# Optimization experiments

Hardware: AMD Instinct MI355X
Metric: run time of the kernel (lower is better)

Reference implementation:

```python
import jax, jax.numpy as jnp
import numpy as np

BETA = 0.25  # commitment loss weight (init kwarg)


def setup_inputs() -> dict:
    key = jax.random.key(0)
    k1, k2 = jax.random.split(key)
    z = jax.random.normal(k1, (16, 256, 32, 32), dtype=jnp.float32)
    embedding = jax.random.normal(k2, (8192, 256), dtype=jnp.float32)
    return {"z": z, "embedding": embedding}


def reference(z, embedding):
    # z: [B, C, H, W]  embedding: [K, C]
    B, C, H, W = z.shape
    zp = jnp.transpose(z, (0, 2, 3, 1))            # [B, H, W, C]
    zf = zp.reshape(-1, C)                          # [N, C]
    # squared euclidean distances via ||z||^2 + ||e||^2 - 2 z.e : [N, K]
    d = (jnp.sum(zf * zf, axis=1, keepdims=True)
         + jnp.sum(embedding * embedding, axis=1)
         - 2.0 * jnp.einsum('nd,kd->nk', zf, embedding))
    min_encoding_indices = jnp.argmin(d, axis=1)    # [N]
    z_q = embedding[min_encoding_indices].reshape(zp.shape)  # [B, H, W, C]
    loss = (BETA * jnp.mean((jax.lax.stop_gradient(z_q) - zp) ** 2)
            + jnp.mean((z_q - jax.lax.stop_gradient(zp)) ** 2))
    # straight-through estimator
    z_q = zp + jax.lax.stop_gradient(z_q - zp)
    z_q = jnp.transpose(z_q, (0, 3, 1, 2))          # back to [B, C, H, W]
    return z_q, loss, min_encoding_indices
```

## Files before the change

kernel.cpp:

```cpp
#include <hip/hip_runtime.h>

typedef unsigned int u32;
typedef unsigned long long u64;

#define C_DIM 256
#define HW 1024
#define N_TOT 16384
#define K_DIM 8192
#define ZQ_SIZE 4194304
#define LOSS_OFF ZQ_SIZE
#define IDX_OFF (ZQ_SIZE + 1)

#define KRANGE 2048
#define MARGIN 2.0f
#define CAP 524288u
#define LCAP 4096u

#define WS_ENORM 0
#define WS_CNT 8192
#define WS_PACKED 16384
#define WS_FIDX 49152
#define WS_LPART 65536
#define WS_LIST 131072
#define WS_ZT32 1179648
#define WS_ZTB16 5373952
#define WS_EB16 7471104

typedef __attribute__((ext_vector_type(4))) float f32x4;
typedef __attribute__((ext_vector_type(8))) __bf16 bf16x8;
typedef __attribute__((ext_vector_type(8))) unsigned short u16x8;

__device__ __forceinline__ void gld_lds16(const void* g, void* l) {
    __builtin_amdgcn_global_load_lds(
        (const __attribute__((address_space(1))) u32*)g,
        (__attribute__((address_space(3))) u32*)l, 16, 0, 0);
}

__device__ __forceinline__ unsigned short f2bf(float f) {
    u32 u = __float_as_uint(f);
    u32 r = (u + 0x7FFFu + ((u >> 16) & 1u)) >> 16;
    return (unsigned short)r;
}

__global__ __launch_bounds__(256) void k_prep_e(const float* __restrict__ e,
                                                unsigned short* __restrict__ eb,
                                                float* __restrict__ enorm1) {
    int w = threadIdx.x >> 6, l = threadIdx.x & 63;
    int row = blockIdx.x * 4 + w;
    const float4 v = *reinterpret_cast<const float4*>(e + (size_t)row * C_DIM + l * 4);
    float s = v.x * v.x + v.y * v.y + v.z * v.z + v.w * v.w;
    #pragma unroll
    for (int off = 32; off; off >>= 1) s += __shfl_xor(s, off, 64);
    if (l == 0) enorm1[row] = s + 1024.0f;
    ushort4 h;
    h.x = f2bf(v.x); h.y = f2bf(v.y); h.z = f2bf(v.z); h.w = f2bf(v.w);
    *reinterpret_cast<ushort4*>(eb + (size_t)row * C_DIM + l * 4) = h;
}

__global__ __launch_bounds__(256) void k_prep_z(const float* __restrict__ z,
                                                float* __restrict__ zt32,
                                                unsigned short* __restrict__ ztb) {
    int bid = blockIdx.x;
    int b = bid >> 7;
    int hwt = (bid >> 3) & 15;
    int ct = bid & 7;
    int t = threadIdx.x;
    __shared__ float tile[32][65];
    #pragma unroll
    for (int p = 0; p < 8; ++p) {
        int cl = p * 4 + (t >> 6), hl = t & 63;
        tile[cl][hl] = z[((size_t)b << 18) + ((size_t)(ct * 32 + cl) << 10) + hwt * 64 + hl];
    }
    __syncthreads();
    int hl = t & 63, cg = t >> 6;
    int n = (b << 10) + hwt * 64 + hl;
    float v[8];
    #pragma unroll
    for (int j = 0; j < 8; ++j) v[j] = tile[cg * 8 + j][hl];
    size_t base = (size_t)n * C_DIM + ct * 32 + cg * 8;
    *reinterpret_cast<float4*>(zt32 + base) = make_float4(v[0], v[1], v[2], v[3]);
    *reinterpret_cast<float4*>(zt32 + base + 4) = make_float4(v[4], v[5], v[6], v[7]);
    u16x8 h;
    #pragma unroll
    for (int j = 0; j < 8; ++j) h[j] = f2bf(v[j]);
    *reinterpret_cast<u16x8*>(ztb + base) = h;
}

__global__ __launch_bounds__(256, 1) void k_screen(const unsigned short* __restrict__ zt,
                                                   const unsigned short* __restrict__ et,
                                                   const float* __restrict__ enorm1,
                                                   u32* __restrict__ cnt,
                                                   uint2* __restrict__ list) {
    __shared__ __align__(16) char lds[50704];
    char* Ab2 = lds;
    char* Bb = lds + 32768;

    int logical = (blockIdx.x & 7) * 64 + (blockIdx.x >> 3);
    const int ks = logical >> 7;
    const int rowtile = logical & 127;
    const int n0 = rowtile * 128;
    const int kbase = ks * KRANGE;

    const int tid = threadIdx.x;
    const int l = tid & 63, w = tid >> 6;
    const int wr = w >> 1, wc = w & 1;
    const int ll = l & 15, lh = l >> 4;

    #pragma unroll
    for (int j = 0; j < 8; ++j) {
        int Y = (w * 8 + j) * 1024 + l * 16;
        int row = Y >> 8;
        int slot = (Y >> 4) & 15;
        const char* src = (const char*)zt + (((size_t)(n0 + row)) << 9) + 256
                          + ((slot ^ (row & 7)) << 4);
        gld_lds16(src, Ab2 + (w * 8 + j) * 1024);
    }

    const char* srcB[2];
    char* dstB[2];
    #pragma unroll
    for (int j = 0; j < 2; ++j) {
        int D = w * 128 + j * 64 + l;
        int rB = D >> 2;
        int sB = (D & 3) ^ ((rB >> 1) & 3);
        srcB[j] = (const char*)et + ((size_t)(kbase + rB) << 9) + (sB << 4);
        dstB[j] = Bb + (w * 128 + j * 64) * 16;
    }
    int bfrOff[4];
    #pragma unroll
    for (int kf = 0; kf < 4; ++kf) {
        int row = wc * 64 + kf * 16 + ll;
        bfrOff[kf] = (row * 4 + (lh ^ ((row >> 1) & 3))) * 16;
    }
    int a2off[4], rx2[4];
    #pragma unroll
    for (int mf = 0; mf < 4; ++mf) {
        int row = wr * 64 + mf * 16 + ll;
        a2off[mf] = row * 256;
        rx2[mf] = row & 7;
    }

    gld_lds16(srcB[0], dstB[0]);
    gld_lds16(srcB[1], dstB[1]);

    const char* abase = (const char*)zt + (((size_t)(n0 + wr * 64 + ll)) << 9) + lh * 16;
    bf16x8 afr[4][4];
    #pragma unroll
    for (int mf = 0; mf < 4; ++mf)
        #pragma unroll
        for (int q = 0; q < 4; ++q)
            afr[mf][q] = *reinterpret_cast<const bf16x8*>(abase + mf * 8192 + q * 64);

    f32x4 acc[4][4];
    #pragma unroll
    for (int a = 0; a < 4; ++a)
        #pragma unroll
        for (int b = 0; b < 4; ++b) acc[a][b] = (f32x4){0.f, 0.f, 0.f, 0.f};
    float m1[16], m2[16];
    #pragma unroll
    for (int s = 0; s < 16; ++s) { m1[s] = 3.4e38f; m2[s] = 3.4e38f; }

    __syncthreads();

    for (int it = 0; it < 16; ++it) {
        float en[4];
        #pragma unroll
        for (int kf = 0; kf < 4; ++kf)
            en[kf] = enorm1[kbase + it * 128 + wc * 64 + kf * 16 + ll];

        #pragma unroll
        for (int cs = 0; cs < 8; ++cs) {
            const int p = cs & 1;
            if (it < 15 || cs < 7) {
                const size_t koff = (size_t)it * 65536 + ((cs == 7) ? 65536 : (cs + 1) * 64);
                gld_lds16(srcB[0] + koff, dstB[0] + (p ^ 1) * 8192);
                gld_lds16(srcB[1] + koff, dstB[1] + (p ^ 1) * 8192);
            }
            bf16x8 bfr[4];
            #pragma unroll
            for (int kf = 0; kf < 4; ++kf)
                bfr[kf] = *reinterpret_cast<const bf16x8*>(Bb + p * 8192 + bfrOff[kf]);
            bf16x8 af[4];
            #pragma unroll
            for (int mf = 0; mf < 4; ++mf) {
                if (cs < 4)
                    af[mf] = afr[mf][cs];
                else
                    af[mf] = *reinterpret_cast<const bf16x8*>(
                        Ab2 + a2off[mf] + ((((cs - 4) * 4 + lh) ^ rx2[mf]) << 4));
            }
            __builtin_amdgcn_s_setprio(1);
            #pragma unroll
            for (int mf = 0; mf < 4; ++mf)
                #pragma unroll
                for (int kf = 0; kf < 4; ++kf)
                    acc[mf][kf] = __builtin_amdgcn_mfma_f32_16x16x32_bf16(
                        af[mf], bfr[kf], acc[mf][kf], 0, 0, 0);
            __builtin_amdgcn_s_setprio(0);

            if (cs == 7) {
                #pragma unroll
                for (int kf = 0; kf < 4; ++kf) {
                    const u32 kcol = (u32)(kbase + it * 128 + wc * 64 + kf * 16 + ll);
                    #pragma unroll
                    for (int mf = 0; mf < 4; ++mf) {
                        #pragma unroll
                        for (int r = 0; r < 4; ++r) {
                            float d = fmaf(-2.0f, acc[mf][kf][r], en[kf]);
                            float df = __uint_as_float((__float_as_uint(d) & 0xFFFFE000u) | kcol);
                            const int s2 = mf * 4 + r;
                            float t = fmaxf(m1[s2], df);
                            m2[s2] = fminf(m2[s2], t);
                            m1[s2] = fminf(m1[s2], df);
                            acc[mf][kf][r] = 0.0f;
                        }
                    }
                }
            }
            __syncthreads();
        }
    }

    float rowm[16];
    #pragma unroll
    for (int s = 0; s < 16; ++s) rowm[s] = m1[s];
    #pragma unroll
    for (int m = 1; m <= 8; m <<= 1)
        #pragma unroll
        for (int s = 0; s < 16; ++s)
            rowm[s] = fminf(rowm[s], __shfl_xor(rowm[s], m, 64));

    float* LDSrm = (float*)(lds + 49152);
    float* LDSrmF = (float*)(lds + 50176);
    u32* ccnt = (u32*)(lds + 50688);
    u32* gbase = (u32*)(lds + 50692);
    uint2* cbuf = (uint2*)lds;

    if (ll == 0) {
        #pragma unroll
        for (int s = 0; s < 16; ++s) {
            int row_local = wr * 64 + (s >> 2) * 16 + lh * 4 + (s & 3);
            LDSrm[row_local * 2 + wc] = rowm[s];
        }
    }
    if (tid == 0) *ccnt = 0;
    __syncthreads();
    if (tid < 128)
        LDSrmF[tid] = fminf(LDSrm[tid * 2], LDSrm[tid * 2 + 1]);
    __syncthreads();

    #pragma unroll
    for (int s = 0; s < 16; ++s) {
        int row_local = wr * 64 + (s >> 2) * 16 + lh * 4 + (s & 3);
        float rm = __uint_as_float(__float_as_uint(LDSrmF[row_local]) & 0xFFFFE000u);
        float d1 = __uint_as_float(__float_as_uint(m1[s]) & 0xFFFFE000u);
        if (d1 <= rm + MARGIN) {
            u32 pos = atomicAdd(ccnt, 1u);
            uint2 ent = make_uint2((u32)(n0 + row_local), __float_as_uint(m1[s]) & 8191u);
            if (pos < LCAP) cbuf[pos] = ent;
            else { u32 gp = atomicAdd(cnt, 1u); if (gp < CAP) list[gp] = ent; }
        }
        float d2 = __uint_as_float(__float_as_uint(m2[s]) & 0xFFFFE000u);
        if (d2 <= rm + MARGIN) {
            for (int it2 = 0; it2 < 16; ++it2) {
                #pragma unroll
                for (int kf = 0; kf < 4; ++kf) {
                    u32 k = (u32)(kbase + it2 * 128 + wc * 64 + kf * 16 + ll);
                    u32 pos = atomicAdd(ccnt, 1u);
                    uint2 ent = make_uint2((u32)(n0 + row_local), k);
                    if (pos < LCAP) cbuf[pos] = ent;
                    else { u32 gp = atomicAdd(cnt, 1u); if (gp < CAP) list[gp] = ent; }
                }
            }
        }
    }
    __syncthreads();
    if (tid == 0) {
        u32 total = *ccnt; if (total > LCAP) total = LCAP;
        *gbase = atomicAdd(cnt, total);
    }
    __syncthreads();
    u32 total = *ccnt; if (total > LCAP) total = LCAP;
    u32 gb = *gbase;
    for (u32 i = tid; i < total; i += 256) {
        u32 gp = gb + i;
        if (gp < CAP) list[gp] = cbuf[i];
    }
}

__global__ __launch_bounds__(256) void k_exact(const float* __restrict__ zt32,
                                               const float* __restrict__ e,
                                               const float* __restrict__ enorm1,
                                               const u32* __restrict__ cnt,
                                               const uint2* __restrict__ list,
                                               u64* __restrict__ packed) {
    const int nw = gridDim.x * 4;
    const int wid = blockIdx.x * 4 + (threadIdx.x >> 6);
    const int l = threadIdx.x & 63;
    u32 total = *cnt;
    if (total > CAP) total = CAP;
    for (u32 i = wid; i < total; i += nw) {
        uint2 c = list[i];
        const float4 zv = *reinterpret_cast<const float4*>(zt32 + (size_t)c.x * C_DIM + l * 4);
        const float4 ev = *reinterpret_cast<const float4*>(e + (size_t)c.y * C_DIM + l * 4);
        float s = zv.x * ev.x + zv.y * ev.y + zv.z * ev.z + zv.w * ev.w;
        #pragma unroll
        for (int off = 32; off; off >>= 1) s += __shfl_xor(s, off, 64);
        if (l == 0) {
            float d = fmaf(-2.0f, s, enorm1[c.y]);
            u32 ub = __float_as_uint(d);
            ub = (ub & 0x80000000u) ? ~ub : (ub | 0x80000000u);
            u64 key = ((u64)ub << 32) | (u64)c.y;
            atomicMin(packed + c.x, key);
        }
    }
}

__global__ __launch_bounds__(256) void k_fin(const u64* __restrict__ packed,
                                             int* __restrict__ fidx,
                                             float* __restrict__ out_idx) {
    int n = blockIdx.x * 256 + threadIdx.x;
    if (n >= N_TOT) return;
    u32 kk = (u32)(packed[n] & 0xFFFFFFFFull);
    if (kk > 8191u) kk = 0u;
    fidx[n] = (int)kk;
    out_idx[n] = (float)kk;
}

#define GBLOCKS 2048
__global__ __launch_bounds__(256) void k_gather(const float* __restrict__ z,
                                                const float* __restrict__ e,
                                                const int* __restrict__ fidx,
                                                float* __restrict__ zq,
                                                float* __restrict__ lpart) {
    float s = 0.0f;
    for (int i = blockIdx.x * 256 + threadIdx.x; i < ZQ_SIZE; i += GBLOCKS * 256) {
        int bb = i >> 18;
        int c = (i >> 10) & 255;
        int hw = i & 1023;
        int n = (bb << 10) | hw;
        float q = e[(size_t)fidx[n] * C_DIM + c];
        float zv = z[i];
        zq[i] = q;
        float d = q - zv;
        s = fmaf(d, d, s);
    }
    #pragma unroll
    for (int off = 32; off; off >>= 1) s += __shfl_xor(s, off, 64);
    __shared__ float wsum[4];
    int lane = threadIdx.x & 63, w = threadIdx.x >> 6;
    if (lane == 0) wsum[w] = s;
    __syncthreads();
    if (threadIdx.x == 0) lpart[blockIdx.x] = wsum[0] + wsum[1] + wsum[2] + wsum[3];
}

__global__ __launch_bounds__(256) void k_loss(const float* __restrict__ lpart,
                                              float* __restrict__ out_loss) {
    float s = 0.0f;
    for (int i = threadIdx.x; i < GBLOCKS; i += 256) s += lpart[i];
    #pragma unroll
    for (int off = 32; off; off >>= 1) s += __shfl_xor(s, off, 64);
    __shared__ float wsum[4];
    int lane = threadIdx.x & 63, w = threadIdx.x >> 6;
    if (lane == 0) wsum[w] = s;
    __syncthreads();
    if (threadIdx.x == 0)
        out_loss[0] = (wsum[0] + wsum[1] + wsum[2] + wsum[3]) * (1.25f / (float)ZQ_SIZE);
}

extern "C" void kernel_launch(void* const* d_in, const int* in_sizes, int n_in,
                              void* d_out, int out_size, void* d_ws, size_t ws_size,
                              hipStream_t stream) {
    const float* z = (const float*)d_in[0];
    const float* e = (const float*)d_in[1];
    float* out = (float*)d_out;
    float* ws = (float*)d_ws;

    float* enorm1 = ws + WS_ENORM;
    u32* cnt = (u32*)(ws + WS_CNT);
    u64* packed = (u64*)(ws + WS_PACKED);
    int* fidx = (int*)(ws + WS_FIDX);
    float* lpart = ws + WS_LPART;
    uint2* list = (uint2*)(ws + WS_LIST);
    float* zt32 = ws + WS_ZT32;
    unsigned short* ztb = (unsigned short*)(ws + WS_ZTB16);
    unsigned short* eb = (unsigned short*)(ws + WS_EB16);

    hipMemsetAsync(cnt, 0, sizeof(u32), stream);
    hipMemsetAsync(packed, 0xFF, (size_t)N_TOT * sizeof(u64), stream);

    k_prep_e<<<dim3(K_DIM / 4), dim3(256), 0, stream>>>(e, eb, enorm1);
    k_prep_z<<<dim3(2048), dim3(256), 0, stream>>>(z, zt32, ztb);
    k_screen<<<dim3(512), dim3(256), 0, stream>>>(ztb, eb, enorm1, cnt, list);
    k_exact<<<dim3(1024), dim3(256), 0, stream>>>(zt32, e, enorm1, cnt, list, packed);
    k_fin<<<dim3(64), dim3(256), 0, stream>>>(packed, fidx, out + IDX_OFF);
    k_gather<<<dim3(GBLOCKS), dim3(256), 0, stream>>>(z, e, fidx, out, lpart);
    k_loss<<<dim3(1), dim3(256), 0, stream>>>(lpart, out + LOSS_OFF);
}
```

Measured before the change: 239.9 us.

## Switch screening GEMM from bf16 to fp8 e4m3 with wider candidate margin

Quantizes z and the codebook to fp8 e4m3, storing them in a permuted byte layout, and runs the candidate-screening GEMM with fp8 MFMA instead of bf16. The goal is to halve the operand bytes and raise MFMA throughput, with all of A now staged in LDS and launch bounds allowing two blocks per CU. Because fp8 is less accurate, the screening margin goes from 2 to 8, which may send more candidates to the exact fp32 refinement kernel and could overflow the list capacity.

```diff
diff --git a/kernel.cpp b/kernel.cpp
--- a/kernel.cpp
+++ b/kernel.cpp
@@ -12,7 +12,7 @@
 #define IDX_OFF (ZQ_SIZE + 1)
 
 #define KRANGE 2048
-#define MARGIN 2.0f
+#define MARGIN 8.0f
 #define CAP 524288u
 #define LCAP 4096u
 
@@ -23,12 +23,11 @@
 #define WS_LPART 65536
 #define WS_LIST 131072
 #define WS_ZT32 1179648
-#define WS_ZTB16 5373952
-#define WS_EB16 7471104
+#define WS_ZT8 5373952
+#define WS_EB8 6422528
 
 typedef __attribute__((ext_vector_type(4))) float f32x4;
-typedef __attribute__((ext_vector_type(8))) __bf16 bf16x8;
-typedef __attribute__((ext_vector_type(8))) unsigned short u16x8;
+typedef __attribute__((ext_vector_type(2))) long i64x2;
 
 __device__ __forceinline__ void gld_lds16(const void* g, void* l) {
     __builtin_amdgcn_global_load_lds(
@@ -36,14 +35,24 @@
         (__attribute__((address_space(3))) u32*)l, 16, 0, 0);
 }
 
-__device__ __forceinline__ unsigned short f2bf(float f) {
-    u32 u = __float_as_uint(f);
-    u32 r = (u + 0x7FFFu + ((u >> 16) & 1u)) >> 16;
-    return (unsigned short)r;
-}
+__device__ __forceinline__ u32 f2e4m3(float x) {
+    u32 b = __float_as_uint(x);
+    u32 s = (b >> 24) & 0x80u;
+    float a = __uint_as_float(b & 0x7FFFFFFFu);
+    if (a >= 464.0f) return s | 0x7Eu;
+    if (a < 0.015625f) {
+        int q = __float2int_rn(a * 512.0f);
+        return s | (u32)q;
+    }
+    u32 m = b & 0x7FFFFFFFu;
+    m += 0x7FFFFu + ((m >> 20) & 1u);
+    u32 e = ((m >> 23) & 0xFFu) - 127u + 7u;
+    return s | (e << 3) | ((m >> 20) & 7u);
+}
+
 
 __global__ __launch_bounds__(256) void k_prep_e(const float* __restrict__ e,
-                                                unsigned short* __restrict__ eb,
+                                                unsigned char* __restrict__ eb8,
                                                 float* __restrict__ enorm1) {
     int w = threadIdx.x >> 6, l = threadIdx.x & 63;
     int row = blockIdx.x * 4 + w;
@@ -52,14 +61,14 @@
     #pragma unroll
     for (int off = 32; off; off >>= 1) s += __shfl_xor(s, off, 64);
     if (l == 0) enorm1[row] = s + 1024.0f;
-    ushort4 h;
-    h.x = f2bf(v.x); h.y = f2bf(v.y); h.z = f2bf(v.z); h.w = f2bf(v.w);
-    *reinterpret_cast<ushort4*>(eb + (size_t)row * C_DIM + l * 4) = h;
+    int p = ((l >> 4) << 6) + (((l >> 1) & 3) << 4) + (((l >> 3) & 1) << 3) + ((l & 1) << 2);
+    u32 pk = f2e4m3(v.x) | (f2e4m3(v.y) << 8) | (f2e4m3(v.z) << 16) | (f2e4m3(v.w) << 24);
+    *reinterpret_cast<u32*>(eb8 + (size_t)row * C_DIM + p) = pk;
 }
 
 __global__ __launch_bounds__(256) void k_prep_z(const float* __restrict__ z,
                                                 float* __restrict__ zt32,
-                                                unsigned short* __restrict__ ztb) {
+                                                unsigned char* __restrict__ zt8) {
     int bid = blockIdx.x;
     int b = bid >> 7;
     int hwt = (bid >> 3) & 15;
@@ -80,19 +89,20 @@
     size_t base = (size_t)n * C_DIM + ct * 32 + cg * 8;
     *reinterpret_cast<float4*>(zt32 + base) = make_float4(v[0], v[1], v[2], v[3]);
     *reinterpret_cast<float4*>(zt32 + base + 4) = make_float4(v[4], v[5], v[6], v[7]);
-    u16x8 h;
-    #pragma unroll
-    for (int j = 0; j < 8; ++j) h[j] = f2bf(v[j]);
-    *reinterpret_cast<u16x8*>(ztb + base) = h;
-}
-
-__global__ __launch_bounds__(256, 1) void k_screen(const unsigned short* __restrict__ zt,
-                                                   const unsigned short* __restrict__ et,
+    u64 pk = 0;
+    #pragma unroll
+    for (int j = 0; j < 8; ++j) pk |= (u64)f2e4m3(v[j]) << (8 * j);
+    int p0 = ((ct >> 1) << 6) + (cg << 4) + ((ct & 1) << 3);
+    *reinterpret_cast<u64*>(zt8 + (size_t)n * C_DIM + p0) = pk;
+}
+
+__global__ __launch_bounds__(256, 2) void k_screen(const unsigned char* __restrict__ zt8,
+                                                   const unsigned char* __restrict__ eb8,
                                                    const float* __restrict__ enorm1,
                                                    u32* __restrict__ cnt,
                                                    uint2* __restrict__ list) {
     __shared__ __align__(16) char lds[50704];
-    char* Ab2 = lds;
+    char* Ab = lds;
     char* Bb = lds + 32768;
 
     int logical = (blockIdx.x & 7) * 64 + (blockIdx.x >> 3);
@@ -108,58 +118,52 @@
 
     #pragma unroll
     for (int j = 0; j < 8; ++j) {
-        int Y = (w * 8 + j) * 1024 + l * 16;
-        int row = Y >> 8;
-        int slot = (Y >> 4) & 15;
-        const char* src = (const char*)zt + (((size_t)(n0 + row)) << 9) + 256
-                          + ((slot ^ (row & 7)) << 4);
-        gld_lds16(src, Ab2 + (w * 8 + j) * 1024);
+        int unit = (w * 8 + j) * 64 + l;
+        int row = unit >> 4;
+        int slot = unit & 15;
+        const char* src = (const char*)zt8 + (((size_t)(n0 + row)) << 8)
+                          + ((slot ^ (row & 15)) << 4);
+        gld_lds16(src, Ab + (w * 8 + j) * 1024);
     }
 
     const char* srcB[2];
     char* dstB[2];
     #pragma unroll
     for (int j = 0; j < 2; ++j) {
-        int D = w * 128 + j * 64 + l;
-        int rB = D >> 2;
-        int sB = (D & 3) ^ ((rB >> 1) & 3);
-        srcB[j] = (const char*)et + ((size_t)(kbase + rB) << 9) + (sB << 4);
-        dstB[j] = Bb + (w * 128 + j * 64) * 16;
+        int unit = j * 256 + w * 64 + l;
+        int rB = unit >> 2;
+        int sB = unit & 3;
+        int sw = (rB ^ (rB >> 2)) & 3;
+        srcB[j] = (const char*)eb8 + ((size_t)(kbase + rB) << 8) + ((sB ^ sw) << 4);
+        dstB[j] = Bb + (j * 256 + w * 64) * 16;
+    }
+
+    int aoff[4], rxA[4];
+    #pragma unroll
+    for (int mf = 0; mf < 4; ++mf) {
+        int row = wr * 64 + mf * 16 + ll;
+        aoff[mf] = row * 256;
+        rxA[mf] = row & 15;
     }
     int bfrOff[4];
     #pragma unroll
     for (int kf = 0; kf < 4; ++kf) {
         int row = wc * 64 + kf * 16 + ll;
-        bfrOff[kf] = (row * 4 + (lh ^ ((row >> 1) & 3))) * 16;
-    }
-    int a2off[4], rx2[4];
-    #pragma unroll
-    for (int mf = 0; mf < 4; ++mf) {
-        int row = wr * 64 + mf * 16 + ll;
-        a2off[mf] = row * 256;
-        rx2[mf] = row & 7;
-    }
+        int sw = (row ^ (row >> 2)) & 3;
+        bfrOff[kf] = row * 64 + ((lh ^ sw) << 4);
+    }
+
+    f32x4 acc[4][4];
+    #pragma unroll
+    for (int a = 0; a < 4; ++a)
+        #pragma unroll
+        for (int b = 0; b < 4; ++b) acc[a][b] = (f32x4){0.f, 0.f, 0.f, 0.f};
+    float m1[16], m2[16];
+    #pragma unroll
+    for (int s = 0; s < 16; ++s) { m1[s] = 3.4e38f; m2[s] = 3.4e38f; }
 
     gld_lds16(srcB[0], dstB[0]);
     gld_lds16(srcB[1], dstB[1]);
-
-    const char* abase = (const char*)zt + (((size_t)(n0 + wr * 64 + ll)) << 9) + lh * 16;
-    bf16x8 afr[4][4];
-    #pragma unroll
-    for (int mf = 0; mf < 4; ++mf)
-        #pragma unroll
-        for (int q = 0; q < 4; ++q)
-            afr[mf][q] = *reinterpret_cast<const bf16x8*>(abase + mf * 8192 + q * 64);
-
-    f32x4 acc[4][4];
-    #pragma unroll
-    for (int a = 0; a < 4; ++a)
-        #pragma unroll
-        for (int b = 0; b < 4; ++b) acc[a][b] = (f32x4){0.f, 0.f, 0.f, 0.f};
-    float m1[16], m2[16];
-    #pragma unroll
-    for (int s = 0; s < 16; ++s) { m1[s] = 3.4e38f; m2[s] = 3.4e38f; }
-
     __syncthreads();
 
     for (int it = 0; it < 16; ++it) {
@@ -169,36 +173,38 @@
             en[kf] = enorm1[kbase + it * 128 + wc * 64 + kf * 16 + ll];
 
         #pragma unroll
-        for (int cs = 0; cs < 8; ++cs) {
-            const int p = cs & 1;
-            if (it < 15 || cs < 7) {
-                const size_t koff = (size_t)it * 65536 + ((cs == 7) ? 65536 : (cs + 1) * 64);
+        for (int t = 0; t < 4; ++t) {
+            const int p = t & 1;
+            if (it < 15 || t < 3) {
+                const int nw = it * 4 + t + 1;
+                const size_t koff = (size_t)(nw >> 2) * 32768 + (size_t)((nw & 3) * 64);
                 gld_lds16(srcB[0] + koff, dstB[0] + (p ^ 1) * 8192);
                 gld_lds16(srcB[1] + koff, dstB[1] + (p ^ 1) * 8192);
             }
-            bf16x8 bfr[4];
+            i64x2 av[4], bv[4];
+            #pragma unroll
+            for (int mf = 0; mf < 4; ++mf)
+                av[mf] = *reinterpret_cast<const i64x2*>(
+                    Ab + aoff[mf] + (((t * 4 + lh) ^ rxA[mf]) << 4));
             #pragma unroll
             for (int kf = 0; kf < 4; ++kf)
-                bfr[kf] = *reinterpret_cast<const bf16x8*>(Bb + p * 8192 + bfrOff[kf]);
-            bf16x8 af[4];
-            #pragma unroll
-            for (int mf = 0; mf < 4; ++mf) {
-                if (cs < 4)
-                    af[mf] = afr[mf][cs];
-                else
-                    af[mf] = *reinterpret_cast<const bf16x8*>(
-                        Ab2 + a2off[mf] + ((((cs - 4) * 4 + lh) ^ rx2[mf]) << 4));
-            }
+                bv[kf] = *reinterpret_cast<const i64x2*>(Bb + p * 8192 + bfrOff[kf]);
             __builtin_amdgcn_s_setprio(1);
             #pragma unroll
             for (int mf = 0; mf < 4; ++mf)
                 #pragma unroll
                 for (int kf = 0; kf < 4; ++kf)
-                    acc[mf][kf] = __builtin_amdgcn_mfma_f32_16x16x32_bf16(
-                        af[mf], bfr[kf], acc[mf][kf], 0, 0, 0);
+                    acc[mf][kf] = __builtin_amdgcn_mfma_f32_16x16x32_fp8_fp8(
+                        av[mf].x, bv[kf].x, acc[mf][kf], 0, 0, 0);
+            #pragma unroll
+            for (int mf = 0; mf < 4; ++mf)
+                #pragma unroll
+                for (int kf = 0; kf < 4; ++kf)
+                    acc[mf][kf] = __builtin_amdgcn_mfma_f32_16x16x32_fp8_fp8(
+                        av[mf].y, bv[kf].y, acc[mf][kf], 0, 0, 0);
             __builtin_amdgcn_s_setprio(0);
 
-            if (cs == 7) {
+            if (t == 3) {
                 #pragma unroll
                 for (int kf = 0; kf < 4; ++kf) {
                     const u32 kcol = (u32)(kbase + it * 128 + wc * 64 + kf * 16 + ll);
@@ -209,8 +215,8 @@
                             float d = fmaf(-2.0f, acc[mf][kf][r], en[kf]);
                             float df = __uint_as_float((__float_as_uint(d) & 0xFFFFE000u) | kcol);
                             const int s2 = mf * 4 + r;
-                            float t = fmaxf(m1[s2], df);
-                            m2[s2] = fminf(m2[s2], t);
+                            float tt = fmaxf(m1[s2], df);
+                            m2[s2] = fminf(m2[s2], tt);
                             m1[s2] = fminf(m1[s2], df);
                             acc[mf][kf][r] = 0.0f;
                         }
@@ -383,15 +389,15 @@
     float* lpart = ws + WS_LPART;
     uint2* list = (uint2*)(ws + WS_LIST);
     float* zt32 = ws + WS_ZT32;
-    unsigned short* ztb = (unsigned short*)(ws + WS_ZTB16);
-    unsigned short* eb = (unsigned short*)(ws + WS_EB16);
+    unsigned char* zt8 = (unsigned char*)(ws + WS_ZT8);
+    unsigned char* eb8 = (unsigned char*)(ws + WS_EB8);
 
     hipMemsetAsync(cnt, 0, sizeof(u32), stream);
     hipMemsetAsync(packed, 0xFF, (size_t)N_TOT * sizeof(u64), stream);
 
-    k_prep_e<<<dim3(K_DIM / 4), dim3(256), 0, stream>>>(e, eb, enorm1);
-    k_prep_z<<<dim3(2048), dim3(256), 0, stream>>>(z, zt32, ztb);
-    k_screen<<<dim3(512), dim3(256), 0, stream>>>(ztb, eb, enorm1, cnt, list);
+    k_prep_e<<<dim3(K_DIM / 4), dim3(256), 0, stream>>>(e, eb8, enorm1);
+    k_prep_z<<<dim3(2048), dim3(256), 0, stream>>>(z, zt32, zt8);
+    k_screen<<<dim3(512), dim3(256), 0, stream>>>(zt8, eb8, enorm1, cnt, list);
     k_exact<<<dim3(1024), dim3(256), 0, stream>>>(zt32, e, enorm1, cnt, list, packed);
     k_fin<<<dim3(64), dim3(256), 0, stream>>>(packed, fidx, out + IDX_OFF);
     k_gather<<<dim3(GBLOCKS), dim3(256), 0, stream>>>(z, e, fidx, out, lpart);
```

Result: slower. 329.7 us (+37.4%).
